# Kernel tuning notes

Hardware: AMD Instinct MI355X
Metric: run time of the kernel (lower is better)

## Reference

```python
import jax, jax.numpy as jnp
import numpy as np

B, S, HID = 2, 2048, 2048
NH, NKV, HD = 16, 4, 128
ROT = 64            # head_dim * partial_rotary_factor
WINDOW = 512        # sliding_window_size
ROPE_BASE = 10000.0


def setup_inputs() -> dict:
    key = jax.random.key(0)
    ks = jax.random.split(key, 5)
    scale = 0.02
    return {
        "hidden_states": jax.random.normal(ks[0], (B, S, HID), jnp.float32),
        "Wq": jax.random.normal(ks[1], (NH * HD, HID), jnp.float32) * scale,
        "Wk": jax.random.normal(ks[2], (NKV * HD, HID), jnp.float32) * scale,
        "Wv": jax.random.normal(ks[3], (NKV * HD, HID), jnp.float32) * scale,
        "Wo": jax.random.normal(ks[4], (HID, NH * HD), jnp.float32) * scale,
    }


def _rope_cos_sin(seq_len, dtype):
    inv_freq = 1.0 / (ROPE_BASE ** (jnp.arange(0, ROT, 2, dtype=jnp.float32) / ROT))
    t = jnp.arange(seq_len, dtype=jnp.float32)
    freqs = t[:, None] * inv_freq[None, :]          # [S, ROT/2]
    emb = jnp.concatenate([freqs, freqs], axis=-1)   # [S, ROT]
    return jnp.cos(emb).astype(dtype), jnp.sin(emb).astype(dtype)


def _rotate_half(x):
    x1, x2 = x[..., : x.shape[-1] // 2], x[..., x.shape[-1] // 2:]
    return jnp.concatenate([-x2, x1], axis=-1)


def reference(hidden_states, Wq, Wk, Wv, Wo):
    b, s, _ = hidden_states.shape
    n_rep = NH // NKV

    q = (hidden_states @ Wq.T).reshape(b, s, NH, HD).transpose(0, 2, 1, 3)    # [B,NH,S,HD]
    k = (hidden_states @ Wk.T).reshape(b, s, NKV, HD).transpose(0, 2, 1, 3)   # [B,NKV,S,HD]
    v = (hidden_states @ Wv.T).reshape(b, s, NKV, HD).transpose(0, 2, 1, 3)

    # partial rotary embedding on the first ROT dims
    cos, sin = _rope_cos_sin(s, q.dtype)   # [S, ROT]
    cos = cos[None, None]                  # broadcast over batch, heads
    sin = sin[None, None]
    q_rot, q_pass = q[..., :ROT], q[..., ROT:]
    k_rot, k_pass = k[..., :ROT], k[..., ROT:]
    q_rot = q_rot * cos + _rotate_half(q_rot) * sin
    k_rot = k_rot * cos + _rotate_half(k_rot) * sin
    q = jnp.concatenate([q_rot, q_pass], axis=-1)
    k = jnp.concatenate([k_rot, k_pass], axis=-1)

    # GQA: repeat kv heads
    k = jnp.repeat(k, n_rep, axis=1)   # [B,NH,S,HD]
    v = jnp.repeat(v, n_rep, axis=1)

    scores = jnp.einsum("bhqd,bhkd->bhqk", q, k) / jnp.sqrt(jnp.asarray(HD, q.dtype))

    # sliding-window causal mask: allow j in [i-WINDOW+1, i]
    i = jnp.arange(s)[:, None]
    j = jnp.arange(s)[None, :]
    allowed = (j <= i) & (j > i - WINDOW)
    scores = jnp.where(allowed[None, None], scores, -jnp.inf)

    attn = jax.nn.softmax(scores.astype(jnp.float32), axis=-1).astype(q.dtype)
    out = jnp.einsum("bhqk,bhkd->bhqd", attn, v)          # [B,NH,S,HD]
    out = out.transpose(0, 2, 1, 3).reshape(b, s, NH * HD)
    return out @ Wo.T
```

## Files before the change

### kernel.cpp

```cpp
#include <hip/hip_runtime.h>
#include <cstdint>
#include <cstddef>

typedef __bf16 bf16;
typedef __attribute__((ext_vector_type(8))) __bf16 bf16x8;
typedef __attribute__((ext_vector_type(4))) __bf16 bf16x4;
typedef __attribute__((ext_vector_type(4))) float f32x4;
typedef __attribute__((ext_vector_type(4))) short s16x4;

#define S_LEN   2048
#define WIN     512
#define NH_Q    16
#define NH_KV   4
#define HD_     128
#define NTOK    4096

#if defined(__has_builtin)
#if __has_builtin(__builtin_amdgcn_mfma_f32_16x16x16bf16_1k)
#define HAVE_MFMA16 1
#endif
#endif
#ifndef HAVE_MFMA16
#define HAVE_MFMA16 0
#endif

#define WAIT_VM40  0x8F78
#define WAIT_VM20  0x4F74
#define WAIT_VM0   0x0F70
#define WAIT_LGKM0 0xC07F
#define CFENCE() __asm__ __volatile__("" ::: "memory")

__device__ __forceinline__ void async_copy16(const void* g, void* l) {
  __builtin_amdgcn_global_load_lds(
      (const __attribute__((address_space(1))) void*)g,
      (__attribute__((address_space(3))) void*)l, 16, 0, 0);
}

__global__ __launch_bounds__(256)
void cvt_all(const float* __restrict__ hs, const float* __restrict__ wq,
             const float* __restrict__ wk, const float* __restrict__ wv,
             const float* __restrict__ wo, bf16* __restrict__ hsb,
             bf16* __restrict__ wqb, bf16* __restrict__ wkb,
             bf16* __restrict__ wvb, bf16* __restrict__ wob) {
  long i = ((long)blockIdx.x * 256 + threadIdx.x) * 4;
  const float* in;
  bf16* out;
  if (i < 8388608)       { in = hs + i;            out = hsb + i; }
  else if (i < 12582912) { in = wq + (i - 8388608); out = wqb + (i - 8388608); }
  else if (i < 13631488) { in = wk + (i - 12582912); out = wkb + (i - 12582912); }
  else if (i < 14680064) { in = wv + (i - 13631488); out = wvb + (i - 13631488); }
  else                   { in = wo + (i - 14680064); out = wob + (i - 14680064); }
  float4 v = *(const float4*)in;
  bf16x4 t = {(bf16)v.x, (bf16)v.y, (bf16)v.z, (bf16)v.w};
  *(bf16x4*)out = t;
}

template <typename OutT>
__global__ __launch_bounds__(256)
void gemm_bt(const bf16* __restrict__ A, const bf16* __restrict__ W,
             OutT* __restrict__ C, int M, int N, int K) {
  __shared__ __align__(16) bf16 As[2][128 * 32];
  __shared__ __align__(16) bf16 Bs[2][128 * 32];
  const int tid  = threadIdx.x;
  const int wave = tid >> 6, lane = tid & 63;
  const int quad = lane >> 4, l16 = lane & 15;
  const int wm = wave >> 1, wn = wave & 1;
  const int m0 = blockIdx.y * 128, n0 = blockIdx.x * 128;
  const int lrow = lane >> 2;
  const int lcol = (((lane & 3) + ((lane >> 3) & 3)) & 3) * 8;
  const int gfrag = ((quad - ((l16 >> 1) & 3)) & 3) * 8;

  f32x4 acc[4][4];
#pragma unroll
  for (int i = 0; i < 4; ++i)
#pragma unroll
    for (int j = 0; j < 4; ++j) acc[i][j] = (f32x4){0.f, 0.f, 0.f, 0.f};

  auto stage = [&](int buf, int k0) {
#pragma unroll
    for (int it = 0; it < 2; ++it) {
      const int c   = it * 4 + wave;
      const int row = c * 16 + lrow;
      async_copy16(A + (size_t)(m0 + row) * K + k0 + lcol, &As[buf][c * 512]);
      async_copy16(W + (size_t)(n0 + row) * K + k0 + lcol, &Bs[buf][c * 512]);
    }
  };

  stage(0, 0);
  __syncthreads();
  for (int k0 = 0; k0 < K; k0 += 32) {
    const int cur = (k0 >> 5) & 1;
    if (k0 + 32 < K) stage(cur ^ 1, k0 + 32);
    bf16x8 af[4], bfr[4];
#pragma unroll
    for (int mt = 0; mt < 4; ++mt)
      af[mt] = *(const bf16x8*)&As[cur][(wm * 64 + mt * 16 + l16) * 32 + gfrag];
#pragma unroll
    for (int nt = 0; nt < 4; ++nt)
      bfr[nt] = *(const bf16x8*)&Bs[cur][(wn * 64 + nt * 16 + l16) * 32 + gfrag];
#pragma unroll
    for (int mt = 0; mt < 4; ++mt)
#pragma unroll
      for (int nt = 0; nt < 4; ++nt)
        acc[mt][nt] = __builtin_amdgcn_mfma_f32_16x16x32_bf16(
            af[mt], bfr[nt], acc[mt][nt], 0, 0, 0);
    __syncthreads();
  }
#pragma unroll
  for (int mt = 0; mt < 4; ++mt)
#pragma unroll
    for (int nt = 0; nt < 4; ++nt)
#pragma unroll
      for (int r = 0; r < 4; ++r) {
        const int row = m0 + wm * 64 + mt * 16 + quad * 4 + r;
        const int col = n0 + wn * 64 + nt * 16 + l16;
        C[(size_t)row * N + col] = (OutT)acc[mt][nt][r];
      }
}

__global__ __launch_bounds__(448, 4)
void gemm_qkv(const bf16* __restrict__ A, const bf16* __restrict__ Wq,
              const bf16* __restrict__ Wk, const bf16* __restrict__ Wv,
              bf16* __restrict__ Qo, bf16* __restrict__ Ko,
              bf16* __restrict__ Vt) {
  __shared__ __align__(16) bf16 As[3][128 * 32];
  __shared__ __align__(16) bf16 Bs[3][192 * 32];
  __shared__ int ready[3];
  __shared__ int done[3];
  const int tid = threadIdx.x, wave = tid >> 6, lane = tid & 63;
  const int quad = lane >> 4, l16 = lane & 15;
  const int bx = blockIdx.x;
  const int m0 = blockIdx.y * 128;
  if (tid < 3) ready[tid] = 0;
  else if (tid < 6) done[tid - 3] = 0;
  __syncthreads();
  volatile int* vready = ready;
  volatile int* vdone  = done;
  const int R = 64;

  if (wave == 6) {
    const int lrow = lane >> 2;
    const int lcol = (((lane & 3) + ((lane >> 3) & 3)) & 3) * 8;
    const bf16* arow = A + (size_t)(m0 + lrow) * 2048 + lcol;
    const bf16* brow[12];
#pragma unroll
    for (int c = 0; c < 12; ++c) {
      const int n = bx * 192 + c * 16 + lrow;
      brow[c] = (n < 2048 ? Wq + (size_t)n * 2048
               : n < 2560 ? Wk + (size_t)(n - 2048) * 2048
                          : Wv + (size_t)(n - 2560) * 2048) + lcol;
    }
    int slot = 0, pslot = 0, need = 0;
    for (int g = 0; g < R; ++g) {
      if (slot == 0 && g) need += 6;
      while (vdone[slot] < need) __builtin_amdgcn_s_sleep(1);
      const int k0 = g * 32;
#pragma unroll
      for (int c = 0; c < 8; ++c)
        async_copy16(arow + (size_t)c * 16 * 2048 + k0, &As[slot][c * 512]);
#pragma unroll
      for (int c = 0; c < 12; ++c)
        async_copy16(brow[c] + k0, &Bs[slot][c * 512]);
      __builtin_amdgcn_s_waitcnt(WAIT_VM40);
      if (g >= 2) {
        if (lane == 0) vready[pslot] = g - 1;
        pslot = pslot == 2 ? 0 : pslot + 1;
      }
      slot = slot == 2 ? 0 : slot + 1;
    }
    __builtin_amdgcn_s_waitcnt(WAIT_VM20);
    if (lane == 0) vready[pslot] = R - 1;
    pslot = pslot == 2 ? 0 : pslot + 1;
    __builtin_amdgcn_s_waitcnt(WAIT_VM0);
    if (lane == 0) vready[pslot] = R;
    return;
  }

  const int wm = wave / 3, wn = wave % 3;
  const int gfrag = ((quad - ((l16 >> 1) & 3)) & 3) * 8;
  f32x4 acc[4][4];
#pragma unroll
  for (int i = 0; i < 4; ++i)
#pragma unroll
    for (int j = 0; j < 4; ++j) acc[i][j] = (f32x4){0.f, 0.f, 0.f, 0.f};

  int slot = 0;
  for (int g = 0; g < R; ++g) {
    while (vready[slot] < g + 1) __builtin_amdgcn_s_sleep(1);
    CFENCE();
    bf16x8 af[4], bfr[4];
#pragma unroll
    for (int mt = 0; mt < 4; ++mt)
      af[mt] = *(const bf16x8*)&As[slot][(wm * 64 + mt * 16 + l16) * 32 + gfrag];
#pragma unroll
    for (int nt = 0; nt < 4; ++nt)
      bfr[nt] = *(const bf16x8*)&Bs[slot][(wn * 64 + nt * 16 + l16) * 32 + gfrag];
#pragma unroll
    for (int mt = 0; mt < 4; ++mt)
#pragma unroll
      for (int nt = 0; nt < 4; ++nt)
        acc[mt][nt] = __builtin_amdgcn_mfma_f32_16x16x32_bf16(
            af[mt], bfr[nt], acc[mt][nt], 0, 0, 0);
    __builtin_amdgcn_s_waitcnt(WAIT_LGKM0);
    CFENCE();
    if (lane == 0) atomicAdd(&done[slot], 1);
    slot = slot == 2 ? 0 : slot + 1;
  }

  const int cbase = bx * 192 + wn * 64;
  if (cbase < 2560 && (cbase & 127) == 0) {
#pragma unroll
    for (int nt = 0; nt < 2; ++nt) {
      const int d = nt * 16 + l16;
      const float invf = exp2f(-(float)d * 0.41524101186091903f);
#pragma unroll
      for (int mt = 0; mt < 4; ++mt)
#pragma unroll
        for (int r = 0; r < 4; ++r) {
          const int pos = (m0 + wm * 64 + mt * 16 + quad * 4 + r) & (S_LEN - 1);
          float s, c;
          __sincosf((float)pos * invf, &s, &c);
          const float x1 = acc[mt][nt][r], x2 = acc[mt][nt + 2][r];
          acc[mt][nt][r]     = x1 * c - x2 * s;
          acc[mt][nt + 2][r] = x2 * c + x1 * s;
        }
    }
  }
#pragma unroll
  for (int mt = 0; mt < 4; ++mt) {
    const int row0 = m0 + wm * 64 + mt * 16 + quad * 4;
#pragma unroll
    for (int nt = 0; nt < 4; ++nt) {
      const int col16 = cbase + nt * 16;
      if (col16 < 2048) {
#pragma unroll
        for (int r = 0; r < 4; ++r)
          Qo[(size_t)(row0 + r) * 2048 + col16 + l16] = (bf16)acc[mt][nt][r];
      } else if (col16 < 2560) {
#pragma unroll
        for (int r = 0; r < 4; ++r)
          Ko[(size_t)(row0 + r) * 512 + col16 - 2048 + l16] = (bf16)acc[mt][nt][r];
      } else {
        const int colv = col16 + l16 - 2560;
        const int b = row0 >> 11, s0 = row0 & (S_LEN - 1);
        bf16x4 t = {(bf16)acc[mt][nt][0], (bf16)acc[mt][nt][1],
                    (bf16)acc[mt][nt][2], (bf16)acc[mt][nt][3]};
        *(bf16x4*)(Vt + ((size_t)(b * NH_KV + (colv >> 7)) * HD_ + (colv & 127))
                        * S_LEN + s0) = t;
      }
    }
  }
}

#define KS_STRIDE 136
#define VT_STRIDE 72

__global__ __launch_bounds__(256)
void attn_kernel(const bf16* __restrict__ Qg, const bf16* __restrict__ Kg,
                 const bf16* __restrict__ Vtg, bf16* __restrict__ Og) {
  __shared__ __align__(16) bf16 Ks[64 * KS_STRIDE];
  __shared__ __align__(16) bf16 Vt[128 * VT_STRIDE];
#if !HAVE_MFMA16
  __shared__ __align__(16) bf16 Pb[4][16 * 72];
#endif
  const int tid  = threadIdx.x;
  const int wave = tid >> 6, lane = tid & 63;
  const int quad = lane >> 4, l16 = lane & 15;
  const int qt = blockIdx.x, h = blockIdx.y, b = blockIdx.z;
  const int kv = h >> 2;
  const int q0 = qt * 64;
  const int tok0 = b * S_LEN;
  const float scale = 0.08838834764831845f;
  const int q = q0 + wave * 16 + l16;

  bf16x8 qf[4];
  {
    const bf16* qp = Qg + (size_t)(tok0 + q) * (NH_Q * HD_) + h * HD_ + quad * 8;
#pragma unroll
    for (int kb = 0; kb < 4; ++kb) qf[kb] = *(const bf16x8*)(qp + kb * 32);
  }

  f32x4 o[8];
#pragma unroll
  for (int dt = 0; dt < 8; ++dt) o[dt] = (f32x4){0.f, 0.f, 0.f, 0.f};
  float m_run = -__builtin_inff(), l_run = 0.f;

  int kt_begin = q0 - WIN;
  if (kt_begin < 0) kt_begin = 0;
  const int kt_end = q0 + 64;
  const bf16* vt_base = Vtg + (size_t)(b * NH_KV + kv) * HD_ * S_LEN;

  for (int kt = kt_begin; kt < kt_end; kt += 64) {
    __syncthreads();
#pragma unroll
    for (int it = 0; it < 4; ++it) {
      int vid = tid + it * 256;
      int key = vid >> 4, dblk = vid & 15;
      bf16x8 v = *(const bf16x8*)(Kg + (size_t)(tok0 + kt + key) * (NH_KV * HD_)
                                  + kv * HD_ + dblk * 8);
      *(bf16x8*)&Ks[key * KS_STRIDE + dblk * 8] = v;
    }
#pragma unroll
    for (int it = 0; it < 4; ++it) {
      int vid = tid + it * 256;
      int d = vid >> 3, kblk = vid & 7;
      bf16x8 v = *(const bf16x8*)(vt_base + (size_t)d * S_LEN + kt + kblk * 8);
      *(bf16x8*)&Vt[d * VT_STRIDE + kblk * 8] = v;
    }
    __syncthreads();

    f32x4 st[4];
#pragma unroll
    for (int nt = 0; nt < 4; ++nt) {
      f32x4 acc = (f32x4){0.f, 0.f, 0.f, 0.f};
#pragma unroll
      for (int kb = 0; kb < 4; ++kb) {
        bf16x8 kf = *(const bf16x8*)&Ks[(nt * 16 + l16) * KS_STRIDE + kb * 32 + quad * 8];
        acc = __builtin_amdgcn_mfma_f32_16x16x32_bf16(kf, qf[kb], acc, 0, 0, 0);
      }
      st[nt] = acc;
    }
#pragma unroll
    for (int nt = 0; nt < 4; ++nt)
#pragma unroll
      for (int r = 0; r < 4; ++r) {
        int key = kt + nt * 16 + quad * 4 + r;
        bool ok = (key <= q) && (key > q - WIN);
        st[nt][r] = ok ? st[nt][r] * scale : -__builtin_inff();
      }
    float mx = -__builtin_inff();
#pragma unroll
    for (int nt = 0; nt < 4; ++nt)
#pragma unroll
      for (int r = 0; r < 4; ++r) mx = fmaxf(mx, st[nt][r]);
    mx = fmaxf(mx, __shfl_xor(mx, 16, 64));
    mx = fmaxf(mx, __shfl_xor(mx, 32, 64));
    float mnew = fmaxf(m_run, mx);
    float msub = (mnew == -__builtin_inff()) ? 0.f : mnew;
    float alpha = __expf(m_run - msub);
    m_run = mnew;
    float p[4][4], psum = 0.f;
#pragma unroll
    for (int nt = 0; nt < 4; ++nt)
#pragma unroll
      for (int r = 0; r < 4; ++r) {
        p[nt][r] = __expf(st[nt][r] - msub);
        psum += p[nt][r];
      }
    psum += __shfl_xor(psum, 16, 64);
    psum += __shfl_xor(psum, 32, 64);
    l_run = l_run * alpha + psum;
#pragma unroll
    for (int dt = 0; dt < 8; ++dt) o[dt] *= alpha;

#if HAVE_MFMA16
    s16x4 pb[4];
#pragma unroll
    for (int nt = 0; nt < 4; ++nt)
#pragma unroll
      for (int r = 0; r < 4; ++r) {
        union { __bf16 h; short s; } u;
        u.h = (bf16)p[nt][r];
        pb[nt][r] = u.s;
      }
#pragma unroll
    for (int dt = 0; dt < 8; ++dt)
#pragma unroll
      for (int nt = 0; nt < 4; ++nt) {
        s16x4 vf = *(const s16x4*)&Vt[(dt * 16 + l16) * VT_STRIDE + nt * 16 + quad * 4];
        o[dt] = __builtin_amdgcn_mfma_f32_16x16x16bf16_1k(vf, pb[nt], o[dt], 0, 0, 0);
      }
#else
#pragma unroll
    for (int nt = 0; nt < 4; ++nt) {
      bf16x4 t;
#pragma unroll
      for (int r = 0; r < 4; ++r) t[r] = (bf16)p[nt][r];
      *(bf16x4*)&Pb[wave][l16 * 72 + nt * 16 + quad * 4] = t;
    }
    __syncthreads();
    bf16x8 pf[2];
    pf[0] = *(const bf16x8*)&Pb[wave][l16 * 72 + quad * 8];
    pf[1] = *(const bf16x8*)&Pb[wave][l16 * 72 + 32 + quad * 8];
#pragma unroll
    for (int dt = 0; dt < 8; ++dt)
#pragma unroll
      for (int kb = 0; kb < 2; ++kb) {
        bf16x8 vf = *(const bf16x8*)&Vt[(dt * 16 + l16) * VT_STRIDE + kb * 32 + quad * 8];
        o[dt] = __builtin_amdgcn_mfma_f32_16x16x32_bf16(vf, pf[kb], o[dt], 0, 0, 0);
      }
#endif
  }

  float inv = 1.f / l_run;
  __syncthreads();
#pragma unroll
  for (int dt = 0; dt < 8; ++dt) {
    bf16x4 t;
#pragma unroll
    for (int r = 0; r < 4; ++r) t[r] = (bf16)(o[dt][r] * inv);
    *(bf16x4*)&Ks[(wave * 16 + l16) * KS_STRIDE + dt * 16 + quad * 4] = t;
  }
  __syncthreads();
#pragma unroll
  for (int it = 0; it < 4; ++it) {
    int idx = tid + it * 256;
    int row = idx >> 4, chunk = idx & 15;
    bf16x8 v = *(const bf16x8*)&Ks[row * KS_STRIDE + chunk * 8];
    *(bf16x8*)(Og + (size_t)(tok0 + q0 + row) * (NH_Q * HD_) + h * HD_ + chunk * 8) = v;
  }
}

extern "C" void kernel_launch(void* const* d_in, const int* in_sizes, int n_in,
                              void* d_out, int out_size, void* d_ws, size_t ws_size,
                              hipStream_t stream) {
  const float* hs = (const float*)d_in[0];
  const float* Wq = (const float*)d_in[1];
  const float* Wk = (const float*)d_in[2];
  const float* Wv = (const float*)d_in[3];
  const float* Wo = (const float*)d_in[4];
  float* out = (float*)d_out;

  char* w = (char*)d_ws;
  bf16* hsb = (bf16*)w; w += (size_t)NTOK * 2048 * 2;
  bf16* wqb = (bf16*)w; w += (size_t)2048 * 2048 * 2;
  bf16* wkb = (bf16*)w; w += (size_t)512 * 2048 * 2;
  bf16* wvb = (bf16*)w; w += (size_t)512 * 2048 * 2;
  bf16* wob = (bf16*)w; w += (size_t)2048 * 2048 * 2;
  bf16* qb  = (bf16*)w; w += (size_t)NTOK * 2048 * 2;
  bf16* kb  = (bf16*)w; w += (size_t)NTOK * 512 * 2;
  bf16* vtb = (bf16*)w; w += (size_t)NTOK * 512 * 2;
  bf16* ab  = hsb;

  cvt_all<<<18874368 / 1024, 256, 0, stream>>>(hs, Wq, Wk, Wv, Wo,
                                               hsb, wqb, wkb, wvb, wob);

  gemm_qkv<<<dim3(16, NTOK / 128), 448, 0, stream>>>(hsb, wqb, wkb, wvb,
                                                     qb, kb, vtb);

  attn_kernel<<<dim3(S_LEN / 64, NH_Q, 2), 256, 0, stream>>>(qb, kb, vtb, ab);

  gemm_bt<float><<<dim3(2048 / 128, NTOK / 128), 256, 0, stream>>>(
      ab, wob, out, NTOK, 2048, 2048);
}
```

Before: 277.3 us.

## Replace output projection GEMM with warp-specialized producer/consumer pipelined kernel

```diff
diff --git a/kernel.cpp b/kernel.cpp
--- a/kernel.cpp
+++ b/kernel.cpp
@@ -24,7 +24,9 @@
 #define HAVE_MFMA16 0
 #endif
 
+#define WAIT_VM48  0xCF70
 #define WAIT_VM40  0x8F78
+#define WAIT_VM24  0x4F78
 #define WAIT_VM20  0x4F74
 #define WAIT_VM0   0x0F70
 #define WAIT_LGKM0 0xC07F
@@ -53,69 +55,6 @@
   float4 v = *(const float4*)in;
   bf16x4 t = {(bf16)v.x, (bf16)v.y, (bf16)v.z, (bf16)v.w};
   *(bf16x4*)out = t;
-}
-
-template <typename OutT>
-__global__ __launch_bounds__(256)
-void gemm_bt(const bf16* __restrict__ A, const bf16* __restrict__ W,
-             OutT* __restrict__ C, int M, int N, int K) {
-  __shared__ __align__(16) bf16 As[2][128 * 32];
-  __shared__ __align__(16) bf16 Bs[2][128 * 32];
-  const int tid  = threadIdx.x;
-  const int wave = tid >> 6, lane = tid & 63;
-  const int quad = lane >> 4, l16 = lane & 15;
-  const int wm = wave >> 1, wn = wave & 1;
-  const int m0 = blockIdx.y * 128, n0 = blockIdx.x * 128;
-  const int lrow = lane >> 2;
-  const int lcol = (((lane & 3) + ((lane >> 3) & 3)) & 3) * 8;
-  const int gfrag = ((quad - ((l16 >> 1) & 3)) & 3) * 8;
-
-  f32x4 acc[4][4];
-#pragma unroll
-  for (int i = 0; i < 4; ++i)
-#pragma unroll
-    for (int j = 0; j < 4; ++j) acc[i][j] = (f32x4){0.f, 0.f, 0.f, 0.f};
-
-  auto stage = [&](int buf, int k0) {
-#pragma unroll
-    for (int it = 0; it < 2; ++it) {
-      const int c   = it * 4 + wave;
-      const int row = c * 16 + lrow;
-      async_copy16(A + (size_t)(m0 + row) * K + k0 + lcol, &As[buf][c * 512]);
-      async_copy16(W + (size_t)(n0 + row) * K + k0 + lcol, &Bs[buf][c * 512]);
-    }
-  };
-
-  stage(0, 0);
-  __syncthreads();
-  for (int k0 = 0; k0 < K; k0 += 32) {
-    const int cur = (k0 >> 5) & 1;
-    if (k0 + 32 < K) stage(cur ^ 1, k0 + 32);
-    bf16x8 af[4], bfr[4];
-#pragma unroll
-    for (int mt = 0; mt < 4; ++mt)
-      af[mt] = *(const bf16x8*)&As[cur][(wm * 64 + mt * 16 + l16) * 32 + gfrag];
-#pragma unroll
-    for (int nt = 0; nt < 4; ++nt)
-      bfr[nt] = *(const bf16x8*)&Bs[cur][(wn * 64 + nt * 16 + l16) * 32 + gfrag];
-#pragma unroll
-    for (int mt = 0; mt < 4; ++mt)
-#pragma unroll
-      for (int nt = 0; nt < 4; ++nt)
-        acc[mt][nt] = __builtin_amdgcn_mfma_f32_16x16x32_bf16(
-            af[mt], bfr[nt], acc[mt][nt], 0, 0, 0);
-    __syncthreads();
-  }
-#pragma unroll
-  for (int mt = 0; mt < 4; ++mt)
-#pragma unroll
-    for (int nt = 0; nt < 4; ++nt)
-#pragma unroll
-      for (int r = 0; r < 4; ++r) {
-        const int row = m0 + wm * 64 + mt * 16 + quad * 4 + r;
-        const int col = n0 + wn * 64 + nt * 16 + l16;
-        C[(size_t)row * N + col] = (OutT)acc[mt][nt][r];
-      }
 }
 
 __global__ __launch_bounds__(448, 4)
@@ -252,6 +191,97 @@
   }
 }
 
+__global__ __launch_bounds__(576)
+void gemm_o(const bf16* __restrict__ A, const bf16* __restrict__ W,
+            float* __restrict__ C) {
+  __shared__ __align__(16) bf16 As[3][128 * 32];
+  __shared__ __align__(16) bf16 Bs[3][256 * 32];
+  __shared__ int ready[3];
+  __shared__ int done[3];
+  const int tid = threadIdx.x, wave = tid >> 6, lane = tid & 63;
+  const int quad = lane >> 4, l16 = lane & 15;
+  const int n0 = blockIdx.x * 256, m0 = blockIdx.y * 128;
+  if (tid < 3) ready[tid] = 0;
+  else if (tid < 6) done[tid - 3] = 0;
+  __syncthreads();
+  volatile int* vready = ready;
+  volatile int* vdone  = done;
+  const int R = 64;
+
+  if (wave == 8) {
+    const int lrow = lane >> 2;
+    const int lcol = (((lane & 3) + ((lane >> 3) & 3)) & 3) * 8;
+    const bf16* arow = A + (size_t)(m0 + lrow) * 2048 + lcol;
+    const bf16* brow = W + (size_t)(n0 + lrow) * 2048 + lcol;
+    int slot = 0, pslot = 0, need = 0;
+    for (int g = 0; g < R; ++g) {
+      if (slot == 0 && g) need += 8;
+      while (vdone[slot] < need) __builtin_amdgcn_s_sleep(1);
+      const int k0 = g * 32;
+#pragma unroll
+      for (int c = 0; c < 8; ++c)
+        async_copy16(arow + (size_t)c * 16 * 2048 + k0, &As[slot][c * 512]);
+#pragma unroll
+      for (int c = 0; c < 16; ++c)
+        async_copy16(brow + (size_t)c * 16 * 2048 + k0, &Bs[slot][c * 512]);
+      __builtin_amdgcn_s_waitcnt(WAIT_VM48);
+      if (g >= 2) {
+        if (lane == 0) vready[pslot] = g - 1;
+        pslot = pslot == 2 ? 0 : pslot + 1;
+      }
+      slot = slot == 2 ? 0 : slot + 1;
+    }
+    __builtin_amdgcn_s_waitcnt(WAIT_VM24);
+    if (lane == 0) vready[pslot] = R - 1;
+    pslot = pslot == 2 ? 0 : pslot + 1;
+    __builtin_amdgcn_s_waitcnt(WAIT_VM0);
+    if (lane == 0) vready[pslot] = R;
+    return;
+  }
+
+  const int wm = wave >> 2, wn = wave & 3;
+  const int gfrag = ((quad - ((l16 >> 1) & 3)) & 3) * 8;
+  f32x4 acc[4][4];
+#pragma unroll
+  for (int i = 0; i < 4; ++i)
+#pragma unroll
+    for (int j = 0; j < 4; ++j) acc[i][j] = (f32x4){0.f, 0.f, 0.f, 0.f};
+
+  int slot = 0;
+  for (int g = 0; g < R; ++g) {
+    while (vready[slot] < g + 1) __builtin_amdgcn_s_sleep(1);
+    CFENCE();
+    bf16x8 af[4], bfr[4];
+#pragma unroll
+    for (int mt = 0; mt < 4; ++mt)
+      af[mt] = *(const bf16x8*)&As[slot][(wm * 64 + mt * 16 + l16) * 32 + gfrag];
+#pragma unroll
+    for (int nt = 0; nt < 4; ++nt)
+      bfr[nt] = *(const bf16x8*)&Bs[slot][(wn * 64 + nt * 16 + l16) * 32 + gfrag];
+#pragma unroll
+    for (int mt = 0; mt < 4; ++mt)
+#pragma unroll
+      for (int nt = 0; nt < 4; ++nt)
+        acc[mt][nt] = __builtin_amdgcn_mfma_f32_16x16x32_bf16(
+            af[mt], bfr[nt], acc[mt][nt], 0, 0, 0);
+    __builtin_amdgcn_s_waitcnt(WAIT_LGKM0);
+    CFENCE();
+    if (lane == 0) atomicAdd(&done[slot], 1);
+    slot = slot == 2 ? 0 : slot + 1;
+  }
+
+#pragma unroll
+  for (int mt = 0; mt < 4; ++mt)
+#pragma unroll
+    for (int nt = 0; nt < 4; ++nt)
+#pragma unroll
+      for (int r = 0; r < 4; ++r) {
+        const int row = m0 + wm * 64 + mt * 16 + quad * 4 + r;
+        const int col = n0 + wn * 64 + nt * 16 + l16;
+        C[(size_t)row * 2048 + col] = acc[mt][nt][r];
+      }
+}
+
 #define KS_STRIDE 136
 #define VT_STRIDE 72
 
@@ -440,6 +470,5 @@
 
   attn_kernel<<<dim3(S_LEN / 64, NH_Q, 2), 256, 0, stream>>>(qb, kb, vtb, ab);
 
-  gemm_bt<float><<<dim3(2048 / 128, NTOK / 128), 256, 0, stream>>>(
-      ab, wob, out, NTOK, 2048, 2048);
-}
+  gemm_o<<<dim3(2048 / 256, NTOK / 128), 576, 0, stream>>>(ab, wob, out);
+}
```

New measurement: 285.6 us. 3.0% more time.
